# Kernel optimization log

Measured on AMD Instinct MI355X. Metric: run time of the kernel, lower is better.

The kernel has to match this reference:

```python
import jax, jax.numpy as jnp
import numpy as np

LN_EPS = 1e-5  # torch.nn.LayerNorm default


def setup_inputs() -> dict:
    key = jax.random.key(0)
    k1, k2 = jax.random.split(key)
    C = 64
    x = jax.random.normal(k1, (1, C, 64, 96, 96), dtype=jnp.float32)
    ln_gamma = jnp.ones((C,), jnp.float32)
    ln_beta = jnp.zeros((C,), jnp.float32)
    # Conv3d(C, 3C, 1, groups=C) -> per-channel scalar weight [3C] and bias [3C]
    conv_w = jax.random.normal(k2, (3 * C,), dtype=jnp.float32) * 0.02
    conv_b = jnp.zeros((3 * C,), jnp.float32)
    return {"x": x, "ln_gamma": ln_gamma, "ln_beta": ln_beta,
            "conv_w": conv_w, "conv_b": conv_b}


def reference(x, ln_gamma, ln_beta, conv_w, conv_b):
    B, C, D, H, W = x.shape
    N = D * H * W
    xf = x.reshape(B, C, N)  # [B, C, N]

    # LayerNorm over the channel dim (module permutes channels last)
    mean = jnp.mean(xf, axis=1, keepdims=True)
    var = jnp.mean(jnp.square(xf - mean), axis=1, keepdims=True)
    y = (xf - mean) * jax.lax.rsqrt(var + LN_EPS)
    y = y * ln_gamma[None, :, None] + ln_beta[None, :, None]

    # grouped 1x1x1 conv: output channel o reads input channel o // 3
    idx = jnp.arange(3 * C) // 3
    y3 = y[:, idx, :] * conv_w[None, :, None] + conv_b[None, :, None]  # [B, 3C, N]
    q, k, v = jnp.split(y3, 3, axis=1)  # each [B, C, N]

    # channel (cross-covariance) attention: logits [B, C, C]
    logits = jnp.einsum('bcn,bkn->bck', q, k) * (C ** -0.5)
    attn = jax.nn.softmax(logits, axis=-1)  # max-subtraction built in
    out = jnp.einsum('bck,bkn->bcn', attn, v).reshape(B, C, D, H, W)
    return x + out
```

## Files before the change

kernel.cpp:

```cpp
#include <hip/hip_runtime.h>

#define NPOS 589824
#define LN_EPS 1e-5f

typedef _Float16 half8 __attribute__((ext_vector_type(8)));
typedef _Float16 half2_t __attribute__((ext_vector_type(2)));
typedef float f32x4 __attribute__((ext_vector_type(4)));
typedef float f32x2 __attribute__((ext_vector_type(2)));

static __device__ __forceinline__ half2_t pk16(float a, float b) {
    return __builtin_bit_cast(half2_t, __builtin_amdgcn_cvt_pkrtz(a, b));
}

#define K1_BLOCKS 576
#define K1_CPB 2
#define YSTR 520


__global__ __launch_bounds__(256, 3) void csa_k1(
    const float* __restrict__ x, const float* __restrict__ lng,
    const float* __restrict__ lnb, float* __restrict__ partials)
{
    __shared__ __align__(16) _Float16 Y[45][YSTR];
    const int tid = threadIdx.x;
    const int lane = tid & 63;
    const int wv = tid >> 6;

    for (int i = tid; i < YSTR; i += 256) {
        Y[43][i] = (_Float16)1.0f;
        Y[44][i] = (_Float16)0.0f;
    }

    f32x4 acc00 = {0.f,0.f,0.f,0.f}, acc01 = acc00, acc10 = acc00, acc11 = acc00;
    const int row = lane & 15;
    const int sub = (lane >> 4) & 3;
    const int kbase = wv * 128 + sub * 8;
    const int r16 = row + 16;
    const int ra1 = (r16 < 22) ? r16 : ((r16 == 22) ? 43 : 44);
    const int rb1 = (r16 < 22) ? (r16 + 21) : ((r16 == 22) ? 43 : 44);
    const int pos0 = blockIdx.x * (K1_CPB * 512);

    for (int ck = 0; ck < K1_CPB; ++ck) {
        const int n0 = pos0 + ck * 512 + tid * 2;
        f32x2 s = {0.f, 0.f}, sq = s;
        half2_t park[43];
        #pragma unroll
        for (int c = 0; c < 64; ++c) {
            f32x2 v = *(const f32x2*)(x + (size_t)c * NPOS + n0);
            s += v; sq += v * v;
            if (c < 43) park[c] = pk16(v[0], v[1]);
        }
        const f32x2 mu = s * (1.f/64.f);
        const f32x2 var = sq * (1.f/64.f) - mu * mu;
        const float rin0 = rsqrtf(fmaxf(var[0], 0.f) + LN_EPS);
        const float rin1 = rsqrtf(fmaxf(var[1], 0.f) + LN_EPS);
        #pragma unroll
        for (int c = 0; c < 43; ++c) {
            const float g = lng[c], b = lnb[c];
            const float rg0 = rin0 * g, rg1 = rin1 * g;
            const float d0 = fmaf(-mu[0], rg0, b);
            const float d1 = fmaf(-mu[1], rg1, b);
            const float y0 = fmaf((float)park[c][0], rg0, d0);
            const float y1 = fmaf((float)park[c][1], rg1, d1);
            *(half2_t*)&Y[c][tid * 2] = pk16(y0, y1);
        }
        __syncthreads();
        #pragma unroll
        for (int s2 = 0; s2 < 4; ++s2) {
            const int kk = kbase + s2 * 32;
            half8 a0 = *(const half8*)&Y[row][kk];
            half8 a1 = *(const half8*)&Y[ra1][kk];
            half8 b0 = *(const half8*)&Y[row + 21][kk];
            half8 b1 = *(const half8*)&Y[rb1][kk];
            acc00 = __builtin_amdgcn_mfma_f32_16x16x32_f16(a0, b0, acc00, 0, 0, 0);
            acc01 = __builtin_amdgcn_mfma_f32_16x16x32_f16(a0, b1, acc01, 0, 0, 0);
            acc10 = __builtin_amdgcn_mfma_f32_16x16x32_f16(a1, b0, acc10, 0, 0, 0);
            acc11 = __builtin_amdgcn_mfma_f32_16x16x32_f16(a1, b1, acc11, 0, 0, 0);
        }
        __syncthreads();
    }
    float* G32 = (float*)&Y[0][0];
    for (int e = tid; e < 1024; e += 256) G32[e] = 0.f;
    __syncthreads();
    const int r0 = (lane >> 4) * 4, c0 = lane & 15;
    #pragma unroll
    for (int r = 0; r < 4; ++r) {
        atomicAdd(&G32[(r0 + r) * 32 + c0],            acc00[r]);
        atomicAdd(&G32[(r0 + r) * 32 + 16 + c0],       acc01[r]);
        atomicAdd(&G32[(16 + r0 + r) * 32 + c0],       acc10[r]);
        atomicAdd(&G32[(16 + r0 + r) * 32 + 16 + c0],  acc11[r]);
    }
    __syncthreads();
    for (int e = tid; e < 1024; e += 256)
        partials[blockIdx.x * 1024 + e] = G32[e];
}

__global__ __launch_bounds__(256) void csa_k2(const float* __restrict__ partials,
                                              float* __restrict__ gfin)
{
    const int e = blockIdx.x * 256 + threadIdx.x;
    float s = 0.f;
    for (int b = 0; b < K1_BLOCKS; ++b) s += partials[b * 1024 + e];
    gfin[e] = s;
}

__global__ void csa_k3(const float* __restrict__ G, const float* __restrict__ cw,
                       const float* __restrict__ cb, float* __restrict__ M,
                       float* __restrict__ betaO)
{
    const int c = threadIdx.x;
    __shared__ float lg[64][65];
    const float wq = cw[c], bq = cb[c];
    const int a = c / 3;
    const float Sa = G[a * 32 + 22];
    float mx = -1e30f;
    #pragma unroll
    for (int k = 0; k < 64; ++k) {
        const float wk = cw[64 + k], bk = cb[64 + k];
        const int b = (64 + k) / 3 - 21;
        const float Gab = G[a * 32 + b];
        const float Sb  = G[22 * 32 + b];
        float lo = 0.125f * (wq * wk * Gab + wq * bk * Sa + bq * wk * Sb
                             + bq * bk * (float)NPOS);
        lg[c][k] = lo;
        mx = fmaxf(mx, lo);
    }
    float sum = 0.f;
    #pragma unroll
    for (int k = 0; k < 64; ++k) {
        float e = expf(lg[c][k] - mx);
        lg[c][k] = e; sum += e;
    }
    const float inv = 1.f / sum;
    float Ml[22];
    #pragma unroll
    for (int m = 0; m < 22; ++m) Ml[m] = 0.f;
    float bacc = 0.f;
    #pragma unroll
    for (int k = 0; k < 64; ++k) {
        const float attn = lg[c][k] * inv;
        const int mm = (128 + k) / 3 - 42;
        Ml[mm] = fmaf(attn, cw[128 + k], Ml[mm]);
        bacc   = fmaf(attn, cb[128 + k], bacc);
    }
    #pragma unroll
    for (int m = 0; m < 22; ++m) M[c * 22 + m] = Ml[m];
    betaO[c] = bacc;
}

__global__ __launch_bounds__(256, 2) void csa_k4(
    const float* __restrict__ x, const float* __restrict__ lng,
    const float* __restrict__ lnb, const float* __restrict__ M,
    const float* __restrict__ betaO, float* __restrict__ out)
{
    const int n0 = (blockIdx.x * 256 + threadIdx.x) * 2;
    f32x2 xv[64];
    f32x2 s = {0.f, 0.f}, sq = s;
    #pragma unroll
    for (int c = 0; c < 64; ++c) {
        f32x2 v = *(const f32x2*)(x + (size_t)c * NPOS + n0);
        xv[c] = v; s += v; sq += v * v;
    }
    const f32x2 mu = s * (1.f/64.f);
    const f32x2 var = sq * (1.f/64.f) - mu * mu;
    const float rin0 = rsqrtf(fmaxf(var[0], 0.f) + LN_EPS);
    const float rin1 = rsqrtf(fmaxf(var[1], 0.f) + LN_EPS);
    f32x2 y[22];
    #pragma unroll
    for (int m = 0; m < 22; ++m) {
        const float g = lng[42 + m], b = lnb[42 + m];
        y[m][0] = fmaf((xv[42 + m][0] - mu[0]) * rin0, g, b);
        y[m][1] = fmaf((xv[42 + m][1] - mu[1]) * rin1, g, b);
    }
    #pragma unroll
    for (int c = 0; c < 64; ++c) {
        const float bb = betaO[c];
        f32x2 a = {bb, bb};
        #pragma unroll
        for (int m = 0; m < 22; ++m) {
            const float w = M[c * 22 + m];
            a[0] = fmaf(w, y[m][0], a[0]);
            a[1] = fmaf(w, y[m][1], a[1]);
        }
        f32x2 o = xv[c] + a;
        __builtin_nontemporal_store(o, (f32x2*)(out + (size_t)c * NPOS + n0));
    }
}

extern "C" void kernel_launch(void* const* d_in, const int* in_sizes, int n_in,
                              void* d_out, int out_size, void* d_ws, size_t ws_size,
                              hipStream_t stream) {
    const float* x   = (const float*)d_in[0];
    const float* lng = (const float*)d_in[1];
    const float* lnb = (const float*)d_in[2];
    const float* cw  = (const float*)d_in[3];
    const float* cb  = (const float*)d_in[4];
    float* out = (float*)d_out;

    float* wsf = (float*)d_ws;
    float* Gf  = wsf;
    float* Mf  = wsf + 1024;
    float* Bf  = wsf + 1024 + 64 * 22;
    float* Pf  = wsf + 4096;

    hipLaunchKernelGGL(csa_k1, dim3(K1_BLOCKS), dim3(256), 0, stream,
                       x, lng, lnb, Pf);
    hipLaunchKernelGGL(csa_k2, dim3(4), dim3(256), 0, stream, Pf, Gf);
    hipLaunchKernelGGL(csa_k3, dim3(1), dim3(64), 0, stream, Gf, cw, cb, Mf, Bf);
    hipLaunchKernelGGL(csa_k4, dim3(NPOS / 512), dim3(256), 0, stream,
                       x, lng, lnb, Mf, Bf, out);
}
```

Before: 152.0 us.

## Process one chunk per block in K1, compact partials, parallelize K2 reduction

```diff
diff --git a/kernel.cpp b/kernel.cpp
--- a/kernel.cpp
+++ b/kernel.cpp
@@ -12,12 +12,11 @@
     return __builtin_bit_cast(half2_t, __builtin_amdgcn_cvt_pkrtz(a, b));
 }
 
-#define K1_BLOCKS 576
-#define K1_CPB 2
+#define K1_BLOCKS 1152
 #define YSTR 520
 
 
-__global__ __launch_bounds__(256, 3) void csa_k1(
+__global__ __launch_bounds__(256, 2) void csa_k1(
     const float* __restrict__ x, const float* __restrict__ lng,
     const float* __restrict__ lnb, float* __restrict__ partials)
 {
@@ -30,6 +29,27 @@
         Y[43][i] = (_Float16)1.0f;
         Y[44][i] = (_Float16)0.0f;
     }
+
+    const int n0 = (blockIdx.x * 256 + tid) * 2;
+    f32x2 xv[64];
+    f32x2 s = {0.f, 0.f}, sq = s;
+    #pragma unroll
+    for (int c = 0; c < 64; ++c) {
+        f32x2 v = *(const f32x2*)(x + (size_t)c * NPOS + n0);
+        xv[c] = v; s += v; sq += v * v;
+    }
+    const f32x2 mu = s * (1.f/64.f);
+    const f32x2 var = sq * (1.f/64.f) - mu * mu;
+    const float rin0 = rsqrtf(fmaxf(var[0], 0.f) + LN_EPS);
+    const float rin1 = rsqrtf(fmaxf(var[1], 0.f) + LN_EPS);
+    #pragma unroll
+    for (int c = 0; c < 43; ++c) {
+        const float g = lng[c], b = lnb[c];
+        const float y0 = fmaf((xv[c][0] - mu[0]) * rin0, g, b);
+        const float y1 = fmaf((xv[c][1] - mu[1]) * rin1, g, b);
+        *(half2_t*)&Y[c][tid * 2] = pk16(y0, y1);
+    }
+    __syncthreads();
 
     f32x4 acc00 = {0.f,0.f,0.f,0.f}, acc01 = acc00, acc10 = acc00, acc11 = acc00;
     const int row = lane & 15;
@@ -38,47 +58,20 @@
     const int r16 = row + 16;
     const int ra1 = (r16 < 22) ? r16 : ((r16 == 22) ? 43 : 44);
     const int rb1 = (r16 < 22) ? (r16 + 21) : ((r16 == 22) ? 43 : 44);
-    const int pos0 = blockIdx.x * (K1_CPB * 512);
-
-    for (int ck = 0; ck < K1_CPB; ++ck) {
-        const int n0 = pos0 + ck * 512 + tid * 2;
-        f32x2 s = {0.f, 0.f}, sq = s;
-        half2_t park[43];
-        #pragma unroll
-        for (int c = 0; c < 64; ++c) {
-            f32x2 v = *(const f32x2*)(x + (size_t)c * NPOS + n0);
-            s += v; sq += v * v;
-            if (c < 43) park[c] = pk16(v[0], v[1]);
-        }
-        const f32x2 mu = s * (1.f/64.f);
-        const f32x2 var = sq * (1.f/64.f) - mu * mu;
-        const float rin0 = rsqrtf(fmaxf(var[0], 0.f) + LN_EPS);
-        const float rin1 = rsqrtf(fmaxf(var[1], 0.f) + LN_EPS);
-        #pragma unroll
-        for (int c = 0; c < 43; ++c) {
-            const float g = lng[c], b = lnb[c];
-            const float rg0 = rin0 * g, rg1 = rin1 * g;
-            const float d0 = fmaf(-mu[0], rg0, b);
-            const float d1 = fmaf(-mu[1], rg1, b);
-            const float y0 = fmaf((float)park[c][0], rg0, d0);
-            const float y1 = fmaf((float)park[c][1], rg1, d1);
-            *(half2_t*)&Y[c][tid * 2] = pk16(y0, y1);
-        }
-        __syncthreads();
-        #pragma unroll
-        for (int s2 = 0; s2 < 4; ++s2) {
-            const int kk = kbase + s2 * 32;
-            half8 a0 = *(const half8*)&Y[row][kk];
-            half8 a1 = *(const half8*)&Y[ra1][kk];
-            half8 b0 = *(const half8*)&Y[row + 21][kk];
-            half8 b1 = *(const half8*)&Y[rb1][kk];
-            acc00 = __builtin_amdgcn_mfma_f32_16x16x32_f16(a0, b0, acc00, 0, 0, 0);
-            acc01 = __builtin_amdgcn_mfma_f32_16x16x32_f16(a0, b1, acc01, 0, 0, 0);
-            acc10 = __builtin_amdgcn_mfma_f32_16x16x32_f16(a1, b0, acc10, 0, 0, 0);
-            acc11 = __builtin_amdgcn_mfma_f32_16x16x32_f16(a1, b1, acc11, 0, 0, 0);
-        }
-        __syncthreads();
-    }
+    #pragma unroll
+    for (int s2 = 0; s2 < 4; ++s2) {
+        const int kk = kbase + s2 * 32;
+        half8 a0 = *(const half8*)&Y[row][kk];
+        half8 a1 = *(const half8*)&Y[ra1][kk];
+        half8 b0 = *(const half8*)&Y[row + 21][kk];
+        half8 b1 = *(const half8*)&Y[rb1][kk];
+        acc00 = __builtin_amdgcn_mfma_f32_16x16x32_f16(a0, b0, acc00, 0, 0, 0);
+        acc01 = __builtin_amdgcn_mfma_f32_16x16x32_f16(a0, b1, acc01, 0, 0, 0);
+        acc10 = __builtin_amdgcn_mfma_f32_16x16x32_f16(a1, b0, acc10, 0, 0, 0);
+        acc11 = __builtin_amdgcn_mfma_f32_16x16x32_f16(a1, b1, acc11, 0, 0, 0);
+    }
+    __syncthreads();
+
     float* G32 = (float*)&Y[0][0];
     for (int e = tid; e < 1024; e += 256) G32[e] = 0.f;
     __syncthreads();
@@ -91,17 +84,26 @@
         atomicAdd(&G32[(16 + r0 + r) * 32 + 16 + c0],  acc11[r]);
     }
     __syncthreads();
-    for (int e = tid; e < 1024; e += 256)
-        partials[blockIdx.x * 1024 + e] = G32[e];
+    for (int e = tid; e < 576; e += 256) {
+        const int r = e / 24, c = e % 24;
+        partials[(size_t)blockIdx.x * 576 + e] = G32[r * 32 + c];
+    }
 }
 
 __global__ __launch_bounds__(256) void csa_k2(const float* __restrict__ partials,
                                               float* __restrict__ gfin)
 {
-    const int e = blockIdx.x * 256 + threadIdx.x;
+    const int tid = threadIdx.x;
+    const int e = blockIdx.x * 16 + (tid >> 4);
+    const int g = tid & 15;
     float s = 0.f;
-    for (int b = 0; b < K1_BLOCKS; ++b) s += partials[b * 1024 + e];
-    gfin[e] = s;
+    for (int b = g; b < K1_BLOCKS; b += 16)
+        s += partials[(size_t)b * 576 + e];
+    s += __shfl_down(s, 8, 16);
+    s += __shfl_down(s, 4, 16);
+    s += __shfl_down(s, 2, 16);
+    s += __shfl_down(s, 1, 16);
+    if (g == 0) gfin[e] = s;
 }
 
 __global__ void csa_k3(const float* __restrict__ G, const float* __restrict__ cw,
@@ -112,14 +114,14 @@
     __shared__ float lg[64][65];
     const float wq = cw[c], bq = cb[c];
     const int a = c / 3;
-    const float Sa = G[a * 32 + 22];
+    const float Sa = G[a * 24 + 22];
     float mx = -1e30f;
     #pragma unroll
     for (int k = 0; k < 64; ++k) {
         const float wk = cw[64 + k], bk = cb[64 + k];
         const int b = (64 + k) / 3 - 21;
-        const float Gab = G[a * 32 + b];
-        const float Sb  = G[22 * 32 + b];
+        const float Gab = G[a * 24 + b];
+        const float Sb  = G[22 * 24 + b];
         float lo = 0.125f * (wq * wk * Gab + wq * bk * Sa + bq * wk * Sb
                              + bq * bk * (float)NPOS);
         lg[c][k] = lo;
@@ -205,7 +207,7 @@
 
     hipLaunchKernelGGL(csa_k1, dim3(K1_BLOCKS), dim3(256), 0, stream,
                        x, lng, lnb, Pf);
-    hipLaunchKernelGGL(csa_k2, dim3(4), dim3(256), 0, stream, Pf, Gf);
+    hipLaunchKernelGGL(csa_k2, dim3(36), dim3(256), 0, stream, Pf, Gf);
     hipLaunchKernelGGL(csa_k3, dim3(1), dim3(64), 0, stream, Gf, cw, cb, Mf, Bf);
     hipLaunchKernelGGL(csa_k4, dim3(NPOS / 512), dim3(256), 0, stream,
                        x, lng, lnb, Mf, Bf, out);
```

Result: faster. 141.8 us (-6.7%).
